# Optimization experiments

Measured on AMD Instinct MI355X. Metric: run time of the kernel, lower is better.

Reference implementation:

```python
import jax, jax.numpy as jnp
import numpy as np

DIM = 25
N_NODES = 20000
N_EDGES = 320000
NFEAT = 300
NHID = 64
NCLASS = 50


def setup_inputs() -> dict:
    key = jax.random.key(0)
    ks = jax.random.split(key, 8)
    s1 = np.sqrt(6.0 / (NFEAT + NHID))
    s2 = np.sqrt(6.0 / (NHID * DIM + NCLASS))
    return {
        "x": jax.random.normal(ks[0], (N_NODES, NFEAT), dtype=jnp.float32),
        "adj_rows": jax.random.randint(ks[1], (DIM, N_EDGES), 0, N_NODES, dtype=jnp.int32),
        "adj_cols": jax.random.randint(ks[2], (DIM, N_EDGES), 0, N_NODES, dtype=jnp.int32),
        "adj_vals": jax.random.uniform(ks[3], (DIM, N_EDGES), dtype=jnp.float32),
        "W1": jax.random.uniform(ks[4], (DIM, NFEAT, NHID), dtype=jnp.float32, minval=-s1, maxval=s1),
        "b1": jnp.zeros((DIM, NHID), dtype=jnp.float32),
        "W2": jax.random.uniform(ks[5], (DIM, NHID * DIM, NCLASS), dtype=jnp.float32, minval=-s2, maxval=s2),
        "b2": jnp.zeros((DIM, NCLASS), dtype=jnp.float32),
    }


def _spmm(rows, cols, vals, sup, n):
    # sparse [n,n] @ dense [n,f] via gather + segment-sum scatter-add
    return jax.ops.segment_sum(vals[:, None] * sup[cols], rows, num_segments=n)


def reference(x, adj_rows, adj_cols, adj_vals, W1, b1, W2, b2):
    n = x.shape[0]
    spmm = jax.vmap(lambda r, c, v, s: _spmm(r, c, v, s, n))
    # layer 1: per-branch dense mm, spmm, bias, relu  -> [DIM, n, NHID]
    sup1 = jnp.einsum("nf,dfh->dnh", x, W1)
    h1 = jax.nn.relu(spmm(adj_rows, adj_cols, adj_vals, sup1) + b1[:, None, :])
    # permute + reshape: concat branch features per node -> [n, DIM*NHID]
    h1cat = jnp.transpose(h1, (1, 0, 2)).reshape(n, -1)
    # layer 2: per-branch dense mm, spmm, bias, relu -> [DIM, n, NCLASS]
    sup2 = jnp.einsum("nk,dkc->dnc", h1cat, W2)
    h2 = jax.nn.relu(spmm(adj_rows, adj_cols, adj_vals, sup2) + b2[:, None, :])
    # max-pool over branches (POOLING='max')
    return jnp.max(h2, axis=0)
```

## Files before the change

kernel.cpp:

```cpp
#include <hip/hip_runtime.h>
#include <hip/hip_bf16.h>
#include <cstdint>
#include <cstddef>

#define DIM 25
#define NN 20000
#define NE 320000
#define NF 300
#define NH 64
#define NC 50
#define K2 (DIM*NH)
#define KP1 320
#define B1T_ROWS 1664
#define B2T_ROWS 1280
#define NBK 79
#define EPB 4096
#define BPB ((NE + EPB - 1) / EPB)
#define FCAP 5632

typedef __attribute__((ext_vector_type(8))) short short8;
typedef __attribute__((ext_vector_type(4))) float floatx4;
typedef __hip_bfloat16 bf16;

static __device__ __forceinline__ unsigned bf16bits(float f) {
    bf16 b = __float2bfloat16(f);
    return (unsigned)*reinterpret_cast<unsigned short*>(&b);
}
static __device__ __forceinline__ float blo(unsigned w) { return __uint_as_float(w << 16); }
static __device__ __forceinline__ float bhi(unsigned w) { return __uint_as_float(w & 0xFFFF0000u); }

static __device__ __forceinline__ void gld16(const void* g, void* l) {
    __builtin_amdgcn_global_load_lds((const __attribute__((address_space(1))) unsigned*)g,
                                     (__attribute__((address_space(3))) unsigned*)l, 16, 0, 0);
}
static __device__ __forceinline__ unsigned lds_off(const void* p) {
    return (unsigned)(size_t)(const __attribute__((address_space(3))) char*)p;
}
#define DSR(dst, a, off) asm volatile("ds_read_b128 %0, %1 offset:" #off : "=v"(dst) : "v"(a))

__global__ void zero_kernel(int* __restrict__ p, int n) {
    int i = blockIdx.x * blockDim.x + threadIdx.x;
    if (i < n) p[i] = 0;
}

__global__ __launch_bounds__(256) void bucket_scatter_kernel(const int* __restrict__ rows,
                                                             const int* __restrict__ cols,
                                                             const float* __restrict__ vals,
                                                             int* __restrict__ gcur,
                                                             unsigned* __restrict__ interE,
                                                             unsigned char* __restrict__ interR) {
    const int d = blockIdx.y;
    const int e0 = blockIdx.x * EPB;
    __shared__ int lh[NBK];
    __shared__ int lo[NBK];
    __shared__ int lbase[NBK];
    __shared__ unsigned entE[EPB];
    __shared__ unsigned short entR[EPB];
    const int tid = threadIdx.x;
    for (int i = tid; i < NBK; i += 256) lh[i] = 0;
    __syncthreads();
    const int* rd = rows + (size_t)d * NE;
    const int* cd = cols + (size_t)d * NE;
    const float* vd = vals + (size_t)d * NE;
    const int e1 = min(e0 + EPB, NE);
    const int ne = e1 - e0;
    for (int i = e0 + tid; i < e1; i += 256)
        atomicAdd(&lh[rd[i] >> 8], 1);
    __syncthreads();
    if (tid == 0) {
        int run = 0;
        for (int b = 0; b < NBK; ++b) { lo[b] = run; run += lh[b]; }
    }
    __syncthreads();
    for (int i = tid; i < NBK; i += 256) {
        lbase[i] = lh[i] ? atomicAdd(&gcur[d * NBK + i], lh[i]) : 0;
        lh[i] = 0;
    }
    __syncthreads();
    for (int i = e0 + tid; i < e1; i += 256) {
        int r = rd[i];
        int b = r >> 8;
        int rank = atomicAdd(&lh[b], 1);
        int pos = lo[b] + rank;
        entE[pos] = (unsigned)cd[i] | (bf16bits(vd[i]) << 16);
        entR[pos] = (unsigned short)r;
    }
    __syncthreads();
    for (int p = tid; p < ne; p += 256) {
        int r = entR[p];
        int b = r >> 8;
        int gpos = lbase[b] + (p - lo[b]);
        if (gpos < FCAP) {
            size_t slot = ((size_t)d * NBK + b) * FCAP + gpos;
            interE[slot] = entE[p];
            interR[slot] = (unsigned char)r;
        }
    }
}

__global__ void bucket_scan_kernel(const int* __restrict__ gcur,
                                   int* __restrict__ offs_b,
                                   int* __restrict__ bcnt,
                                   int* __restrict__ offs) {
    const int d = blockIdx.x;
    if (threadIdx.x != 0) return;
    int run = 0;
    for (int b = 0; b < NBK; ++b) {
        int c = min(gcur[d * NBK + b], FCAP);
        offs_b[d * NBK + b] = run;
        bcnt[d * NBK + b] = c;
        run += c;
    }
    offs[d * (NN + 1) + NN] = run;
}

__global__ __launch_bounds__(256) void csr_finalize_kernel(const unsigned* __restrict__ interE,
                                                           const unsigned char* __restrict__ interR,
                                                           const int* __restrict__ offs_b,
                                                           const int* __restrict__ bcnt,
                                                           int* __restrict__ offs,
                                                           unsigned* __restrict__ sedge) {
    const int d = blockIdx.y;
    const int b = blockIdx.x;
    const int tid = threadIdx.x;
    const int s = offs_b[d * NBK + b];
    const int cnt = bcnt[d * NBK + b];
    const size_t base = ((size_t)d * NBK + b) * FCAP;
    __shared__ int sm[256];
    __shared__ int cur[256];
    __shared__ unsigned lse[FCAP];
    sm[tid] = 0;
    __syncthreads();
    for (int i = tid; i < cnt; i += 256)
        atomicAdd(&sm[interR[base + i]], 1);
    __syncthreads();
    int own = sm[tid];
    for (int off = 1; off < 256; off <<= 1) {
        int t = (tid >= off) ? sm[tid - off] : 0;
        __syncthreads();
        sm[tid] += t;
        __syncthreads();
    }
    int excl = sm[tid] - own;
    int row = (b << 8) + tid;
    if (row < NN) offs[d * (NN + 1) + row] = s + excl;
    cur[tid] = excl;
    __syncthreads();
    for (int i = tid; i < cnt; i += 256) {
        int idx = atomicAdd(&cur[interR[base + i]], 1);
        lse[idx] = interE[base + i];
    }
    __syncthreads();
    unsigned* sed = sedge + (size_t)d * NE;
    for (int t = tid; t < cnt; t += 256)
        sed[s + t] = lse[t];
}

__global__ void pack_x_kernel(const float* __restrict__ x, bf16* __restrict__ xb) {
    int i = blockIdx.x * blockDim.x + threadIdx.x;
    if (i >= NN * KP1) return;
    int n = i / KP1, k = i - n * KP1;
    xb[i] = __float2bfloat16((k < NF) ? x[(size_t)n * NF + k] : 0.f);
}

__global__ void pack_b1_kernel(const float* __restrict__ W1, bf16* __restrict__ b1t) {
    int i = blockIdx.x * blockDim.x + threadIdx.x;
    if (i >= B1T_ROWS * KP1) return;
    int j2 = i / KP1, k = i - j2 * KP1;
    int chunk = j2 >> 9;
    int r = j2 & 511;
    int d = chunk * 8 + (r >> 6);
    float v = 0.f;
    if (d < DIM && k < NF)
        v = W1[(size_t)d * NF * NH + (size_t)k * NH + (r & 63)];
    b1t[i] = __float2bfloat16(v);
}

__global__ void pack_b2_kernel(const float* __restrict__ W2, bf16* __restrict__ b2t) {
    int i = blockIdx.x * blockDim.x + threadIdx.x;
    if (i >= B2T_ROWS * K2) return;
    int r = i / K2, k = i - r * K2;
    float v = 0.f;
    if (r < DIM * NC) {
        int g = r / NC, c = r - g * NC;
        v = W2[(size_t)g * K2 * NC + (size_t)k * NC + c];
    }
    b2t[i] = __float2bfloat16(v);
}

__global__ __launch_bounds__(512, 2) void gemm256_bf16_kernel(const bf16* __restrict__ A, int lda,
                                                              const bf16* __restrict__ BT, int ldb,
                                                              bf16* __restrict__ C,
                                                              int ktiles, int mode, int nvalid) {
    __shared__ unsigned short As[2 * 256 * 64];
    __shared__ unsigned short Bs[2 * 256 * 64];
    const int tid = threadIdx.x;
    const int w = tid >> 6;
    const int l = tid & 63;
    const int MT = (int)gridDim.x;
    const int NT = (int)gridDim.y;
    const int bid = (int)blockIdx.y * MT + (int)blockIdx.x;
    const int pg = 8 * NT;
    const int grp = bid / pg;
    const int rem = bid - grp * pg;
    const int fm = grp * 8;
    const int gm = min(8, MT - fm);
    const int mt = fm + rem % gm;
    const int nt = rem / gm;
    const int m0 = mt * 256, n0 = nt * 256;
    const int wr = w >> 2, wc = w & 3;

    floatx4 acc[8][4] = {};

    const int strow = w * 8 + (l >> 3);
    const int gch = (l & 7) ^ (l >> 3);
    const bf16* pA[4];
    const bf16* pB[4];
    #pragma unroll
    for (int q = 0; q < 4; ++q) {
        pA[q] = A + (size_t)(m0 + q * 64 + strow) * lda + gch * 8;
        pB[q] = BT + (size_t)(n0 + q * 64 + strow) * ldb + gch * 8;
    }
    const unsigned slc0 = (unsigned)(((l >> 4)) ^ (l & 7)) * 16u;
    const unsigned slc1 = (unsigned)((4 + (l >> 4)) ^ (l & 7)) * 16u;
    const unsigned aRow = (unsigned)(wr * 128 + (l & 15)) * 128u;
    const unsigned bRow = (unsigned)(wc * 64 + (l & 15)) * 128u;
    const unsigned ldsA = lds_off(As), ldsB = lds_off(Bs);

    #pragma unroll
    for (int q = 0; q < 4; ++q) { gld16(pA[q], As + q * 4096 + w * 512); pA[q] += 64; }
    #pragma unroll
    for (int q = 0; q < 4; ++q) { gld16(pB[q], Bs + q * 4096 + w * 512); pB[q] += 64; }
    asm volatile("s_waitcnt vmcnt(0)");
    __builtin_amdgcn_sched_barrier(0);
    __builtin_amdgcn_s_barrier();
    __builtin_amdgcn_sched_barrier(0);

    short8 aF[4][2], bF[4][2];
    for (int kt = 0; kt < ktiles; ++kt) {
        const int c = kt & 1;
        const unsigned boff = (unsigned)c * 32768u;
        const unsigned aA0 = ldsA + boff + aRow + slc0;
        const unsigned aA1 = ldsA + boff + aRow + slc1;
        const unsigned bA0 = ldsB + boff + bRow + slc0;
        const unsigned bA1 = ldsB + boff + bRow + slc1;
        unsigned short* nA = As + (c ^ 1) * 16384 + w * 512;
        unsigned short* nB = Bs + (c ^ 1) * 16384 + w * 512;
        const bool stage = (kt + 1 < ktiles);
        DSR(aF[0][0], aA0, 0);    DSR(aF[0][1], aA1, 0);
        DSR(aF[1][0], aA0, 2048); DSR(aF[1][1], aA1, 2048);
        DSR(aF[2][0], aA0, 4096); DSR(aF[2][1], aA1, 4096);
        DSR(aF[3][0], aA0, 6144); DSR(aF[3][1], aA1, 6144);
        DSR(bF[0][0], bA0, 0);    DSR(bF[0][1], bA1, 0);
        DSR(bF[1][0], bA0, 2048); DSR(bF[1][1], bA1, 2048);
        if (stage) {
            gld16(pA[0], nA);         gld16(pA[1], nA + 4096);
            gld16(pA[2], nA + 8192);  gld16(pA[3], nA + 12288);
            pA[0] += 64; pA[1] += 64; pA[2] += 64; pA[3] += 64;
        }
        asm volatile("s_waitcnt lgkmcnt(0)");
        __builtin_amdgcn_sched_barrier(0);
        __builtin_amdgcn_s_setprio(1);
        #pragma unroll
        for (int mf = 0; mf < 4; ++mf)
            #pragma unroll
            for (int nf = 0; nf < 2; ++nf) {
                acc[mf][nf] = __builtin_amdgcn_mfma_f32_16x16x32_bf16(aF[mf][0], bF[nf][0], acc[mf][nf], 0, 0, 0);
                acc[mf][nf] = __builtin_amdgcn_mfma_f32_16x16x32_bf16(aF[mf][1], bF[nf][1], acc[mf][nf], 0, 0, 0);
            }
        __builtin_amdgcn_s_setprio(0);
        __builtin_amdgcn_sched_barrier(0);
        DSR(bF[2][0], bA0, 4096); DSR(bF[2][1], bA1, 4096);
        DSR(bF[3][0], bA0, 6144); DSR(bF[3][1], bA1, 6144);
        if (stage) {
            gld16(pB[0], nB);         gld16(pB[1], nB + 4096);
            gld16(pB[2], nB + 8192);  gld16(pB[3], nB + 12288);
            pB[0] += 64; pB[1] += 64; pB[2] += 64; pB[3] += 64;
        }
        asm volatile("s_waitcnt lgkmcnt(0)");
        __builtin_amdgcn_sched_barrier(0);
        __builtin_amdgcn_s_setprio(1);
        #pragma unroll
        for (int mf = 0; mf < 4; ++mf)
            #pragma unroll
            for (int nf = 2; nf < 4; ++nf) {
                acc[mf][nf] = __builtin_amdgcn_mfma_f32_16x16x32_bf16(aF[mf][0], bF[nf][0], acc[mf][nf], 0, 0, 0);
                acc[mf][nf] = __builtin_amdgcn_mfma_f32_16x16x32_bf16(aF[mf][1], bF[nf][1], acc[mf][nf], 0, 0, 0);
            }
        __builtin_amdgcn_s_setprio(0);
        __builtin_amdgcn_sched_barrier(0);
        DSR(aF[0][0], aA0, 8192);  DSR(aF[0][1], aA1, 8192);
        DSR(aF[1][0], aA0, 10240); DSR(aF[1][1], aA1, 10240);
        DSR(aF[2][0], aA0, 12288); DSR(aF[2][1], aA1, 12288);
        DSR(aF[3][0], aA0, 14336); DSR(aF[3][1], aA1, 14336);
        asm volatile("s_waitcnt lgkmcnt(0)");
        __builtin_amdgcn_sched_barrier(0);
        __builtin_amdgcn_s_setprio(1);
        #pragma unroll
        for (int mf = 0; mf < 4; ++mf)
            #pragma unroll
            for (int nf = 2; nf < 4; ++nf) {
                acc[mf + 4][nf] = __builtin_amdgcn_mfma_f32_16x16x32_bf16(aF[mf][0], bF[nf][0], acc[mf + 4][nf], 0, 0, 0);
                acc[mf + 4][nf] = __builtin_amdgcn_mfma_f32_16x16x32_bf16(aF[mf][1], bF[nf][1], acc[mf + 4][nf], 0, 0, 0);
            }
        __builtin_amdgcn_s_setprio(0);
        __builtin_amdgcn_sched_barrier(0);
        __builtin_amdgcn_s_setprio(1);
        #pragma unroll
        for (int mf = 0; mf < 4; ++mf)
            #pragma unroll
            for (int nf = 0; nf < 2; ++nf) {
                acc[mf + 4][nf] = __builtin_amdgcn_mfma_f32_16x16x32_bf16(aF[mf][0], bF[nf][0], acc[mf + 4][nf], 0, 0, 0);
                acc[mf + 4][nf] = __builtin_amdgcn_mfma_f32_16x16x32_bf16(aF[mf][1], bF[nf][1], acc[mf + 4][nf], 0, 0, 0);
            }
        __builtin_amdgcn_s_setprio(0);
        __builtin_amdgcn_sched_barrier(0);
        if (stage) {
            asm volatile("s_waitcnt vmcnt(0)");
            __builtin_amdgcn_sched_barrier(0);
            __builtin_amdgcn_s_barrier();
            __builtin_amdgcn_sched_barrier(0);
        }
    }
    const int cr = (l >> 4) * 4;
    const int cc = l & 15;
    #pragma unroll
    for (int mf = 0; mf < 8; ++mf) {
        #pragma unroll
        for (int r = 0; r < 4; ++r) {
            int m = m0 + wr * 128 + mf * 16 + cr + r;
            if (m >= NN) continue;
            #pragma unroll
            for (int nf = 0; nf < 4; ++nf) {
                int n = n0 + wc * 64 + nf * 16 + cc;
                if (n >= nvalid) continue;
                if (mode == 1) {
                    int g = n >> 6, h = n & 63;
                    C[(size_t)g * NN * NH + (size_t)m * NH + h] = __float2bfloat16(acc[mf][nf][r]);
                } else {
                    int g = n / NC, cl2 = n - g * NC;
                    C[(size_t)g * NN * NC + (size_t)m * NC + cl2] = __float2bfloat16(acc[mf][nf][r]);
                }
            }
        }
    }
}

__global__ __launch_bounds__(256) void gemm_bf16_kernel(const bf16* __restrict__ A, int lda,
                                                        const bf16* __restrict__ BT, int ldb,
                                                        bf16* __restrict__ C,
                                                        int ksteps, int mode, int nvalid) {
    __shared__ unsigned short As[3 * 128 * 32];
    __shared__ unsigned short Bs[3 * 128 * 32];
    const int tid = threadIdx.x;
    const int wave = tid >> 6;
    const int lane = tid & 63;
    const int mtiles = (int)gridDim.x;
    const int ntiles = (int)gridDim.y;
    const int bid = (int)blockIdx.y * mtiles + (int)blockIdx.x;
    const int per_group = 8 * ntiles;
    const int group = bid / per_group;
    const int rem = bid - group * per_group;
    const int first_m = group * 8;
    const int gm = min(8, mtiles - first_m);
    const int mt = first_m + rem % gm;
    const int nt = rem / gm;
    const int m0 = mt * 128;
    const int n0 = nt * 128;
    const int wm = (wave >> 1) * 64;
    const int wn = (wave & 1) * 64;
    floatx4 acc[4][4] = {};
    const int r0 = tid >> 2;
    const int cg = (tid & 3) ^ ((r0 >> 1) & 3);
    const int q8 = (lane >> 4) * 8;
    const int gq = q8 >> 3;
    unsigned short* lA0 = As + wave * 512;
    unsigned short* lA1 = As + 2048 + wave * 512;
    unsigned short* lB0 = Bs + wave * 512;
    unsigned short* lB1 = Bs + 2048 + wave * 512;
    const bf16* gA0 = A + (size_t)(m0 + r0) * lda + cg * 8;
    const bf16* gA1 = A + (size_t)(m0 + r0 + 64) * lda + cg * 8;
    const bf16* gB0 = BT + (size_t)(n0 + r0) * ldb + cg * 8;
    const bf16* gB1 = BT + (size_t)(n0 + r0 + 64) * ldb + cg * 8;
    int offA[4], offB[4];
    #pragma unroll
    for (int i = 0; i < 4; ++i) {
        int ra = wm + i * 16 + (lane & 15);
        int rb = wn + i * 16 + (lane & 15);
        offA[i] = ra * 32 + ((gq ^ ((ra >> 1) & 3)) << 3);
        offB[i] = rb * 32 + ((gq ^ ((rb >> 1) & 3)) << 3);
    }
    gld16(gA0, lA0); gld16(gA1, lA1); gld16(gB0, lB0); gld16(gB1, lB1);
    if (ksteps > 1) {
        gld16(gA0 + 32, lA0 + 4096); gld16(gA1 + 32, lA1 + 4096);
        gld16(gB0 + 32, lB0 + 4096); gld16(gB1 + 32, lB1 + 4096);
    }
    const bf16* pA0 = gA0 + 64;
    const bf16* pA1 = gA1 + 64;
    const bf16* pB0 = gB0 + 64;
    const bf16* pB1 = gB1 + 64;
    int buf = 0;
    int pbuf = 2;
    for (int ks = 0; ks < ksteps; ++ks) {
        if (ks + 1 < ksteps) asm volatile("s_waitcnt vmcnt(4)" ::: "memory");
        else                 asm volatile("s_waitcnt vmcnt(0)" ::: "memory");
        __builtin_amdgcn_sched_barrier(0);
        __builtin_amdgcn_s_barrier();
        __builtin_amdgcn_sched_barrier(0);
        if (ks + 2 < ksteps) {
            unsigned short* dA0 = lA0 + pbuf * 4096;
            unsigned short* dA1 = lA1 + pbuf * 4096;
            unsigned short* dB0 = lB0 + pbuf * 4096;
            unsigned short* dB1 = lB1 + pbuf * 4096;
            gld16(pA0, dA0); gld16(pA1, dA1); gld16(pB0, dB0); gld16(pB1, dB1);
            pA0 += 32; pA1 += 32; pB0 += 32; pB1 += 32;
            pbuf = (pbuf == 2) ? 0 : pbuf + 1;
        }
        const unsigned short* as = As + buf * 4096;
        const unsigned short* bs = Bs + buf * 4096;
        short8 af[4], bfr[4];
        #pragma unroll
        for (int i = 0; i < 4; ++i) {
            af[i]  = *(const short8*)&as[offA[i]];
            bfr[i] = *(const short8*)&bs[offB[i]];
        }
        #pragma unroll
        for (int i = 0; i < 4; ++i)
            #pragma unroll
            for (int j = 0; j < 4; ++j)
                acc[i][j] = __builtin_amdgcn_mfma_f32_16x16x32_bf16(af[i], bfr[j], acc[i][j], 0, 0, 0);
        buf = (buf == 2) ? 0 : buf + 1;
    }
    const int cr = (lane >> 4) * 4;
    const int cc = lane & 15;
    #pragma unroll
    for (int i = 0; i < 4; ++i) {
        #pragma unroll
        for (int r = 0; r < 4; ++r) {
            int m = m0 + wm + i * 16 + cr + r;
            if (m >= NN) continue;
            #pragma unroll
            for (int j = 0; j < 4; ++j) {
                int n = n0 + wn + j * 16 + cc;
                if (n >= nvalid) continue;
                if (mode == 1) {
                    int g = n >> 6, h = n & 63;
                    C[(size_t)g * NN * NH + (size_t)m * NH + h] = __float2bfloat16(acc[i][j][r]);
                } else {
                    int g = n / NC, c = n - g * NC;
                    C[(size_t)g * NN * NC + (size_t)m * NC + c] = __float2bfloat16(acc[i][j][r]);
                }
            }
        }
    }
}

#define S1EDGE(ew, aL, aH) { \
    unsigned w_ = *(const unsigned*)(supd + ((((ew) & 0xFFFFu) << 7) | hoff)); \
    float v_ = bhi(ew); \
    aL = fmaf(v_, blo(w_), aL); aH = fmaf(v_, bhi(w_), aH); }
#define S1QUAD(q) { S1EDGE((q).x, alo0, ahi0) S1EDGE((q).y, alo1, ahi1) \
                    S1EDGE((q).z, alo0, ahi0) S1EDGE((q).w, alo1, ahi1) }
__global__ __launch_bounds__(256) void spmm1_kernel(const bf16* __restrict__ sup,
                                                    const int* __restrict__ offs,
                                                    const unsigned* __restrict__ sedge,
                                                    const float* __restrict__ b1,
                                                    bf16* __restrict__ h1cat, int d0, int CHk) {
    const int i = blockIdx.x;
    const int g = i % CHk;
    const int nb = i / CHk;
    const int tid = threadIdx.x;
    const int lane = tid & 63;
    const int n = nb * 8 + ((tid >> 6) << 1) + (lane >> 5);
    const int hl = lane & 31;
    const int d = d0 + g;
    const int s = offs[d * (NN + 1) + n];
    const int e = offs[d * (NN + 1) + n + 1];
    const char* supd = (const char*)sup + (size_t)g * NN * NH * 2;
    const unsigned* sed = sedge + (size_t)d * NE;
    const unsigned hoff = (unsigned)hl * 4;
    float alo0 = 0.f, ahi0 = 0.f, alo1 = 0.f, ahi1 = 0.f;
    int j = s;
    const int jal = min(e, (s + 3) & ~3);
    for (; j < jal; ++j) { unsigned e0 = sed[j]; S1EDGE(e0, alo0, ahi0) }
    int nq = (e - j) >> 2;
    if (nq > 0) {
        uint4 q = *(const uint4*)&sed[j];
        for (int t = 1; t < nq; ++t) {
            uint4 qn = *(const uint4*)&sed[j + 4 * t];
            S1QUAD(q)
            q = qn;
        }
        S1QUAD(q)
        j += nq << 2;
    }
    for (; j < e; ++j) { unsigned e0 = sed[j]; S1EDGE(e0, alo0, ahi0) }
    float alo = fmaxf((alo0 + alo1) + b1[d * NH + 2 * hl], 0.f);
    float ahi = fmaxf((ahi0 + ahi1) + b1[d * NH + 2 * hl + 1], 0.f);
    unsigned packed = bf16bits(alo) | (bf16bits(ahi) << 16);
    *(unsigned*)((char*)h1cat + ((size_t)n * K2 + d * NH) * 2 + hoff) = packed;
}

#define S2EDGE(ew, aL, aH) { \
    unsigned w_ = *(const unsigned*)(supd + (((ew) & 0xFFFFu) * 100u + coff)); \
    float v_ = bhi(ew); \
    aL = fmaf(v_, blo(w_), aL); aH = fmaf(v_, bhi(w_), aH); }
#define S2QUAD(q) { S2EDGE((q).x, alo0, ahi0) S2EDGE((q).y, alo1, ahi1) \
                    S2EDGE((q).z, alo0, ahi0) S2EDGE((q).w, alo1, ahi1) }
__global__ __launch_bounds__(256) void spmm2b_kernel(const bf16* __restrict__ sup2,
                                                     const int* __restrict__ offs,
                                                     const unsigned* __restrict__ sedge,
                                                     const float* __restrict__ b2,
                                                     unsigned* __restrict__ h2u) {
    const int i = blockIdx.x;
    const int r = i & 7;
    const int q_ = i >> 3;
    int d, nb;
    if (q_ < 7500) { d = r + 8 * (q_ / 2500); nb = q_ % 2500; }
    else { d = 24; nb = (q_ - 7500) * 8 + r; if (nb >= 2500) return; }
    const int tid = threadIdx.x;
    const int lane = tid & 63;
    const int n = nb * 8 + ((tid >> 6) << 1) + (lane >> 5);
    const int cl = min(lane & 31, 24);
    const unsigned coff = (unsigned)cl * 4;
    const int s = offs[d * (NN + 1) + n];
    const int e = offs[d * (NN + 1) + n + 1];
    const char* supd = (const char*)sup2 + (size_t)d * NN * NC * 2;
    const unsigned* sed = sedge + (size_t)d * NE;
    float alo0 = b2[d * NC + 2 * cl], ahi0 = b2[d * NC + 2 * cl + 1];
    float alo1 = 0.f, ahi1 = 0.f;
    int j = s;
    const int jal = min(e, (s + 3) & ~3);
    for (; j < jal; ++j) { unsigned e0 = sed[j]; S2EDGE(e0, alo0, ahi0) }
    int nq = (e - j) >> 2;
    if (nq > 0) {
        uint4 q = *(const uint4*)&sed[j];
        for (int t = 1; t < nq; ++t) {
            uint4 qn = *(const uint4*)&sed[j + 4 * t];
            S2QUAD(q)
            q = qn;
        }
        S2QUAD(q)
        j += nq << 2;
    }
    for (; j < e; ++j) { unsigned e0 = sed[j]; S2EDGE(e0, alo0, ahi0) }
    float alo = fmaxf(alo0 + alo1, 0.f);
    float ahi = fmaxf(ahi0 + ahi1, 0.f);
    if ((lane & 31) < 25)
        h2u[((size_t)d * NN + n) * 25 + cl] = bf16bits(alo) | (bf16bits(ahi) << 16);
}

__global__ __launch_bounds__(256) void maxk_kernel(const unsigned* __restrict__ h2u,
                                                   float* __restrict__ out) {
    int i = blockIdx.x * blockDim.x + threadIdx.x;
    if (i >= NN * 25) return;
    int n = i / 25, cl = i - n * 25;
    float mlo = 0.f, mhi = 0.f;
    #pragma unroll
    for (int d = 0; d < DIM; ++d) {
        unsigned w = h2u[(size_t)d * NN * 25 + i];
        mlo = fmaxf(mlo, blo(w));
        mhi = fmaxf(mhi, bhi(w));
    }
    *(float2*)&out[(size_t)n * NC + 2 * cl] = make_float2(mlo, mhi);
}

extern "C" void kernel_launch(void* const* d_in, const int* in_sizes, int n_in,
                              void* d_out, int out_size, void* d_ws, size_t ws_size,
                              hipStream_t stream) {
    const float* x    = (const float*)d_in[0];
    const int*   rows = (const int*)d_in[1];
    const int*   cols = (const int*)d_in[2];
    const float* vals = (const float*)d_in[3];
    const float* W1   = (const float*)d_in[4];
    const float* b1   = (const float*)d_in[5];
    const float* W2   = (const float*)d_in[6];
    const float* b2   = (const float*)d_in[7];
    float* out = (float*)d_out;

    char* ws = (char*)d_ws;
    size_t off = 0;
    auto alloc = [&](size_t bytes) {
        void* p = ws + off;
        off += (bytes + 255) & ~(size_t)255;
        return p;
    };
    bf16* supbuf = (bf16*)alloc(sizeof(bf16) * (size_t)DIM * NN * NC);
    bf16* h1cat  = (bf16*)alloc(sizeof(bf16) * (size_t)NN * K2);
    bf16* b1t    = (bf16*)alloc(sizeof(bf16) * (size_t)B1T_ROWS * KP1);
    bf16* b2t    = (bf16*)alloc(sizeof(bf16) * (size_t)B2T_ROWS * K2);
    int*  offs   = (int*)alloc(sizeof(int) * (size_t)DIM * (NN + 1));
    int*  gcur   = (int*)alloc(sizeof(int) * (size_t)DIM * NBK);
    int*  offs_b = (int*)alloc(sizeof(int) * (size_t)DIM * NBK);
    int*  bcnt   = (int*)alloc(sizeof(int) * (size_t)DIM * NBK);
    unsigned* sedge = (unsigned*)alloc(sizeof(unsigned) * (size_t)DIM * NE);

    bf16* sup1 = supbuf;
    bf16* xbf  = supbuf + (size_t)12 * 1024 * 1024;
    bf16* sup2 = supbuf;
    unsigned* interE = (unsigned*)h1cat;
    unsigned char* interR = (unsigned char*)h1cat + (size_t)DIM * NBK * FCAP * 4;
    unsigned* h2u = (unsigned*)h1cat;

    if (off > ws_size) return;

    zero_kernel<<<(DIM * NBK + 255) / 256, 256, 0, stream>>>(gcur, DIM * NBK);
    bucket_scatter_kernel<<<dim3(BPB, DIM), 256, 0, stream>>>(rows, cols, vals, gcur, interE, interR);
    bucket_scan_kernel<<<DIM, 64, 0, stream>>>(gcur, offs_b, bcnt, offs);
    csr_finalize_kernel<<<dim3(NBK, DIM), 256, 0, stream>>>(interE, interR, offs_b, bcnt, offs, sedge);

    pack_x_kernel<<<(NN * KP1 + 255) / 256, 256, 0, stream>>>(x, xbf);
    pack_b1_kernel<<<(B1T_ROWS * KP1 + 255) / 256, 256, 0, stream>>>(W1, b1t);
    pack_b2_kernel<<<(B2T_ROWS * K2 + 255) / 256, 256, 0, stream>>>(W2, b2t);

    const int mtiles128 = (NN + 127) / 128;
    const int mtiles256 = (NN + 255) / 256;

    const int cstart[4] = {0, 8, 16, 24};
    const int csize[4]  = {8, 8, 8, 1};
    const int crow[4]   = {0, 512, 1024, 1536};
    for (int c = 0; c < 3; ++c) {
        gemm256_bf16_kernel<<<dim3(mtiles256, 2), 512, 0, stream>>>(
            xbf, KP1, b1t + (size_t)crow[c] * KP1, KP1, sup1, KP1 / 64, 1, 512);
        spmm1_kernel<<<csize[c] * (NN / 8), 256, 0, stream>>>(
            sup1, offs, sedge, b1, h1cat, cstart[c], csize[c]);
    }
    gemm_bf16_kernel<<<dim3(mtiles128, 1), 256, 0, stream>>>(
        xbf, KP1, b1t + (size_t)crow[3] * KP1, KP1, sup1, KP1 / 32, 1, 64);
    spmm1_kernel<<<csize[3] * (NN / 8), 256, 0, stream>>>(
        sup1, offs, sedge, b1, h1cat, cstart[3], csize[3]);

    gemm256_bf16_kernel<<<dim3(mtiles256, B2T_ROWS / 256), 512, 0, stream>>>(
        h1cat, K2, b2t, K2, sup2, K2 / 64, 2, DIM * NC);
    spmm2b_kernel<<<8 * 7813, 256, 0, stream>>>(sup2, offs, sedge, b2, h2u);
    maxk_kernel<<<(NN * 25 + 255) / 256, 256, 0, stream>>>(h2u, out);
}
```

Baseline: 745.2 us.

## Pad sup2 rows to 52 and split SpMM edges across two half-waves

The layer-2 support buffer is stored with a padded row stride of 52 bf16 so each gathered row can be read with 8-byte loads. Both SpMM kernels now have 16 lanes each load four features per edge, while the two 16-lane halves handle alternating edges and combine their sums with a cross-lane shuffle. This halves the number of lanes per node row and widens each gather, aiming for fewer memory transactions per edge. The cost is a slightly larger workspace, a shuffle reduction, and idle lanes in the layer-2 kernel where 13 lanes cover 50 columns.

```diff
diff --git a/kernel.cpp b/kernel.cpp
--- a/kernel.cpp
+++ b/kernel.cpp
@@ -17,6 +17,7 @@
 #define EPB 4096
 #define BPB ((NE + EPB - 1) / EPB)
 #define FCAP 5632
+#define S2W 52
 
 typedef __attribute__((ext_vector_type(8))) short short8;
 typedef __attribute__((ext_vector_type(4))) float floatx4;
@@ -339,7 +340,7 @@
                     C[(size_t)g * NN * NH + (size_t)m * NH + h] = __float2bfloat16(acc[mf][nf][r]);
                 } else {
                     int g = n / NC, cl2 = n - g * NC;
-                    C[(size_t)g * NN * NC + (size_t)m * NC + cl2] = __float2bfloat16(acc[mf][nf][r]);
+                    C[((size_t)g * NN + m) * S2W + cl2] = __float2bfloat16(acc[mf][nf][r]);
                 }
             }
         }
@@ -448,19 +449,13 @@
                     C[(size_t)g * NN * NH + (size_t)m * NH + h] = __float2bfloat16(acc[i][j][r]);
                 } else {
                     int g = n / NC, c = n - g * NC;
-                    C[(size_t)g * NN * NC + (size_t)m * NC + c] = __float2bfloat16(acc[i][j][r]);
+                    C[((size_t)g * NN + m) * S2W + c] = __float2bfloat16(acc[i][j][r]);
                 }
             }
         }
     }
 }
 
-#define S1EDGE(ew, aL, aH) { \
-    unsigned w_ = *(const unsigned*)(supd + ((((ew) & 0xFFFFu) << 7) | hoff)); \
-    float v_ = bhi(ew); \
-    aL = fmaf(v_, blo(w_), aL); aH = fmaf(v_, bhi(w_), aH); }
-#define S1QUAD(q) { S1EDGE((q).x, alo0, ahi0) S1EDGE((q).y, alo1, ahi1) \
-                    S1EDGE((q).z, alo0, ahi0) S1EDGE((q).w, alo1, ahi1) }
 __global__ __launch_bounds__(256) void spmm1_kernel(const bf16* __restrict__ sup,
                                                     const int* __restrict__ offs,
                                                     const unsigned* __restrict__ sedge,
@@ -472,41 +467,62 @@
     const int tid = threadIdx.x;
     const int lane = tid & 63;
     const int n = nb * 8 + ((tid >> 6) << 1) + (lane >> 5);
-    const int hl = lane & 31;
+    const int sg = (lane >> 4) & 1;
+    const int c = lane & 15;
     const int d = d0 + g;
     const int s = offs[d * (NN + 1) + n];
     const int e = offs[d * (NN + 1) + n + 1];
     const char* supd = (const char*)sup + (size_t)g * NN * NH * 2;
     const unsigned* sed = sedge + (size_t)d * NE;
-    const unsigned hoff = (unsigned)hl * 4;
-    float alo0 = 0.f, ahi0 = 0.f, alo1 = 0.f, ahi1 = 0.f;
-    int j = s;
-    const int jal = min(e, (s + 3) & ~3);
-    for (; j < jal; ++j) { unsigned e0 = sed[j]; S1EDGE(e0, alo0, ahi0) }
-    int nq = (e - j) >> 2;
-    if (nq > 0) {
-        uint4 q = *(const uint4*)&sed[j];
-        for (int t = 1; t < nq; ++t) {
-            uint4 qn = *(const uint4*)&sed[j + 4 * t];
-            S1QUAD(q)
-            q = qn;
-        }
-        S1QUAD(q)
-        j += nq << 2;
-    }
-    for (; j < e; ++j) { unsigned e0 = sed[j]; S1EDGE(e0, alo0, ahi0) }
-    float alo = fmaxf((alo0 + alo1) + b1[d * NH + 2 * hl], 0.f);
-    float ahi = fmaxf((ahi0 + ahi1) + b1[d * NH + 2 * hl + 1], 0.f);
-    unsigned packed = bf16bits(alo) | (bf16bits(ahi) << 16);
-    *(unsigned*)((char*)h1cat + ((size_t)n * K2 + d * NH) * 2 + hoff) = packed;
-}
-
-#define S2EDGE(ew, aL, aH) { \
-    unsigned w_ = *(const unsigned*)(supd + (((ew) & 0xFFFFu) * 100u + coff)); \
-    float v_ = bhi(ew); \
-    aL = fmaf(v_, blo(w_), aL); aH = fmaf(v_, bhi(w_), aH); }
-#define S2QUAD(q) { S2EDGE((q).x, alo0, ahi0) S2EDGE((q).y, alo1, ahi1) \
-                    S2EDGE((q).z, alo0, ahi0) S2EDGE((q).w, alo1, ahi1) }
+    const unsigned boff = (unsigned)c * 8;
+    float a0 = 0.f, a1 = 0.f, a2 = 0.f, a3 = 0.f;
+    const int deg = e - s;
+    const int T = deg >> 1;
+    int j = s + sg;
+    int t = 0;
+    for (; t + 2 <= T; t += 2) {
+        unsigned ew0 = sed[j];
+        unsigned ew1 = sed[j + 2];
+        uint2 w0 = *(const uint2*)(supd + (((ew0 & 0xFFFFu) << 7) | boff));
+        uint2 w1 = *(const uint2*)(supd + (((ew1 & 0xFFFFu) << 7) | boff));
+        float v0 = bhi(ew0), v1 = bhi(ew1);
+        a0 = fmaf(v0, blo(w0.x), a0); a1 = fmaf(v0, bhi(w0.x), a1);
+        a2 = fmaf(v0, blo(w0.y), a2); a3 = fmaf(v0, bhi(w0.y), a3);
+        a0 = fmaf(v1, blo(w1.x), a0); a1 = fmaf(v1, bhi(w1.x), a1);
+        a2 = fmaf(v1, blo(w1.y), a2); a3 = fmaf(v1, bhi(w1.y), a3);
+        j += 4;
+    }
+    for (; t < T; ++t) {
+        unsigned ew0 = sed[j];
+        uint2 w0 = *(const uint2*)(supd + (((ew0 & 0xFFFFu) << 7) | boff));
+        float v0 = bhi(ew0);
+        a0 = fmaf(v0, blo(w0.x), a0); a1 = fmaf(v0, bhi(w0.x), a1);
+        a2 = fmaf(v0, blo(w0.y), a2); a3 = fmaf(v0, bhi(w0.y), a3);
+        j += 2;
+    }
+    if ((deg & 1) && sg == 0) {
+        unsigned ew0 = sed[e - 1];
+        uint2 w0 = *(const uint2*)(supd + (((ew0 & 0xFFFFu) << 7) | boff));
+        float v0 = bhi(ew0);
+        a0 = fmaf(v0, blo(w0.x), a0); a1 = fmaf(v0, bhi(w0.x), a1);
+        a2 = fmaf(v0, blo(w0.y), a2); a3 = fmaf(v0, bhi(w0.y), a3);
+    }
+    a0 += __shfl_xor(a0, 16, 64);
+    a1 += __shfl_xor(a1, 16, 64);
+    a2 += __shfl_xor(a2, 16, 64);
+    a3 += __shfl_xor(a3, 16, 64);
+    if (sg == 0) {
+        float f0 = fmaxf(a0 + b1[d * NH + 4 * c], 0.f);
+        float f1 = fmaxf(a1 + b1[d * NH + 4 * c + 1], 0.f);
+        float f2 = fmaxf(a2 + b1[d * NH + 4 * c + 2], 0.f);
+        float f3 = fmaxf(a3 + b1[d * NH + 4 * c + 3], 0.f);
+        uint2 pk;
+        pk.x = bf16bits(f0) | (bf16bits(f1) << 16);
+        pk.y = bf16bits(f2) | (bf16bits(f3) << 16);
+        *(uint2*)((char*)h1cat + ((size_t)n * K2 + d * NH) * 2 + c * 8) = pk;
+    }
+}
+
 __global__ __launch_bounds__(256) void spmm2b_kernel(const bf16* __restrict__ sup2,
                                                      const int* __restrict__ offs,
                                                      const unsigned* __restrict__ sedge,
@@ -521,33 +537,60 @@
     const int tid = threadIdx.x;
     const int lane = tid & 63;
     const int n = nb * 8 + ((tid >> 6) << 1) + (lane >> 5);
-    const int cl = min(lane & 31, 24);
-    const unsigned coff = (unsigned)cl * 4;
+    const int sg = (lane >> 4) & 1;
+    const int c = min(lane & 15, 12);
+    const unsigned boff = (unsigned)c * 8;
     const int s = offs[d * (NN + 1) + n];
     const int e = offs[d * (NN + 1) + n + 1];
-    const char* supd = (const char*)sup2 + (size_t)d * NN * NC * 2;
+    const char* supd = (const char*)sup2 + (size_t)d * NN * S2W * 2;
     const unsigned* sed = sedge + (size_t)d * NE;
-    float alo0 = b2[d * NC + 2 * cl], ahi0 = b2[d * NC + 2 * cl + 1];
-    float alo1 = 0.f, ahi1 = 0.f;
-    int j = s;
-    const int jal = min(e, (s + 3) & ~3);
-    for (; j < jal; ++j) { unsigned e0 = sed[j]; S2EDGE(e0, alo0, ahi0) }
-    int nq = (e - j) >> 2;
-    if (nq > 0) {
-        uint4 q = *(const uint4*)&sed[j];
-        for (int t = 1; t < nq; ++t) {
-            uint4 qn = *(const uint4*)&sed[j + 4 * t];
-            S2QUAD(q)
-            q = qn;
-        }
-        S2QUAD(q)
-        j += nq << 2;
-    }
-    for (; j < e; ++j) { unsigned e0 = sed[j]; S2EDGE(e0, alo0, ahi0) }
-    float alo = fmaxf(alo0 + alo1, 0.f);
-    float ahi = fmaxf(ahi0 + ahi1, 0.f);
-    if ((lane & 31) < 25)
-        h2u[((size_t)d * NN + n) * 25 + cl] = bf16bits(alo) | (bf16bits(ahi) << 16);
+    float a0 = 0.f, a1 = 0.f, a2 = 0.f, a3 = 0.f;
+    const int deg = e - s;
+    const int T = deg >> 1;
+    int j = s + sg;
+    int t = 0;
+    for (; t + 2 <= T; t += 2) {
+        unsigned ew0 = sed[j];
+        unsigned ew1 = sed[j + 2];
+        uint2 w0 = *(const uint2*)(supd + (ew0 & 0xFFFFu) * 104u + boff);
+        uint2 w1 = *(const uint2*)(supd + (ew1 & 0xFFFFu) * 104u + boff);
+        float v0 = bhi(ew0), v1 = bhi(ew1);
+        a0 = fmaf(v0, blo(w0.x), a0); a1 = fmaf(v0, bhi(w0.x), a1);
+        a2 = fmaf(v0, blo(w0.y), a2); a3 = fmaf(v0, bhi(w0.y), a3);
+        a0 = fmaf(v1, blo(w1.x), a0); a1 = fmaf(v1, bhi(w1.x), a1);
+        a2 = fmaf(v1, blo(w1.y), a2); a3 = fmaf(v1, bhi(w1.y), a3);
+        j += 4;
+    }
+    for (; t < T; ++t) {
+        unsigned ew0 = sed[j];
+        uint2 w0 = *(const uint2*)(supd + (ew0 & 0xFFFFu) * 104u + boff);
+        float v0 = bhi(ew0);
+        a0 = fmaf(v0, blo(w0.x), a0); a1 = fmaf(v0, bhi(w0.x), a1);
+        a2 = fmaf(v0, blo(w0.y), a2); a3 = fmaf(v0, bhi(w0.y), a3);
+        j += 2;
+    }
+    if ((deg & 1) && sg == 0) {
+        unsigned ew0 = sed[e - 1];
+        uint2 w0 = *(const uint2*)(supd + (ew0 & 0xFFFFu) * 104u + boff);
+        float v0 = bhi(ew0);
+        a0 = fmaf(v0, blo(w0.x), a0); a1 = fmaf(v0, bhi(w0.x), a1);
+        a2 = fmaf(v0, blo(w0.y), a2); a3 = fmaf(v0, bhi(w0.y), a3);
+    }
+    a0 += __shfl_xor(a0, 16, 64);
+    a1 += __shfl_xor(a1, 16, 64);
+    a2 += __shfl_xor(a2, 16, 64);
+    a3 += __shfl_xor(a3, 16, 64);
+    if (sg == 0 && (lane & 15) == c) {
+        const size_t row = ((size_t)d * NN + n) * 25;
+        float f0 = fmaxf(a0 + b2[d * NC + 4 * c], 0.f);
+        float f1 = fmaxf(a1 + b2[d * NC + 4 * c + 1], 0.f);
+        h2u[row + 2 * c] = bf16bits(f0) | (bf16bits(f1) << 16);
+        if (c < 12) {
+            float f2 = fmaxf(a2 + b2[d * NC + 4 * c + 2], 0.f);
+            float f3 = fmaxf(a3 + b2[d * NC + 4 * c + 3], 0.f);
+            h2u[row + 2 * c + 1] = bf16bits(f2) | (bf16bits(f3) << 16);
+        }
+    }
 }
 
 __global__ __launch_bounds__(256) void maxk_kernel(const unsigned* __restrict__ h2u,
@@ -585,7 +628,7 @@
         off += (bytes + 255) & ~(size_t)255;
         return p;
     };
-    bf16* supbuf = (bf16*)alloc(sizeof(bf16) * (size_t)DIM * NN * NC);
+    bf16* supbuf = (bf16*)alloc((size_t)DIM * NN * S2W * 2);
     bf16* h1cat  = (bf16*)alloc(sizeof(bf16) * (size_t)NN * K2);
     bf16* b1t    = (bf16*)alloc(sizeof(bf16) * (size_t)B1T_ROWS * KP1);
     bf16* b2t    = (bf16*)alloc(sizeof(bf16) * (size_t)B2T_ROWS * K2);
```

Measured after the change: 756.2 us. No clear change (+1.5%).
